# Optimization experiments

Measured on AMD Instinct MI355X. Metric: run time of the kernel, lower is better.

The kernel has to match this reference:

```python
import jax, jax.numpy as jnp
import numpy as np

B, N, E, F_IN, F_OUT = 2, 50000, 800000, 128, 128


def setup_inputs() -> dict:
    key = jax.random.key(0)
    k1, k2, k3, k4 = jax.random.split(key, 4)
    x = jax.random.normal(k1, (B, N, F_IN), dtype=jnp.float32)
    edge_index = jax.random.randint(k2, (2, E), 0, N, dtype=jnp.int64)
    edge_weight = jax.random.uniform(k3, (E,), dtype=jnp.float32)
    # Linear params (xavier_uniform weight, zero bias)
    limit = float(np.sqrt(6.0 / (F_IN + F_OUT)))
    W = jax.random.uniform(k4, (F_OUT, F_IN), minval=-limit, maxval=limit, dtype=jnp.float32)
    b = jnp.zeros((F_OUT,), dtype=jnp.float32)
    return {"x": x, "edge_index": edge_index, "edge_weight": edge_weight, "W": W, "b": b}


def reference(x, edge_index, edge_weight, W, b):
    src, dst = edge_index[0], edge_index[1]
    num_nodes = x.shape[1]
    # in-degree of dst, clamped to >= 1
    deg = jax.ops.segment_sum(jnp.ones_like(dst, dtype=x.dtype), dst, num_segments=num_nodes)
    deg_inv_sqrt = jnp.clip(deg, 1.0, None) ** -0.5
    norm = deg_inv_sqrt[src] * edge_weight * deg_inv_sqrt[dst]  # [E]

    def aggregate(xb):  # xb: [N, F]
        msg = xb[src] * norm[:, None]  # [E, F] gather + scale
        return jax.ops.segment_sum(msg, dst, num_segments=num_nodes)  # scatter-add

    out = jax.vmap(aggregate)(x)  # [B, N, F]
    return out @ W.T + b
```

## Files before the change

kernel.cpp:

```cpp
#include <hip/hip_runtime.h>
#include <hip/hip_fp16.h>

typedef unsigned int u32;
typedef unsigned short u16;
typedef __attribute__((ext_vector_type(8))) short bf16x8;
typedef __attribute__((ext_vector_type(4))) float f32x4;

#define WS_ALIGN(x) (((x) + 255) & ~(size_t)255)

__device__ inline u16 f2bf(float f) {
    u32 u = __float_as_uint(f);
    u32 r = (u + 0x7fffu + ((u >> 16) & 1u)) >> 16;
    return (u16)r;
}

__global__ void prep_kernel(const float* __restrict__ W, uint2* __restrict__ Wh,
                            int* __restrict__ deg, int N) {
    int t = blockIdx.x * 256 + threadIdx.x;
    if (t < N) deg[t] = 0;
    if (t < 4096) {
        float4 v = ((const float4*)W)[t];
        Wh[t] = make_uint2((u32)f2bf(v.x) | ((u32)f2bf(v.y) << 16),
                           (u32)f2bf(v.z) | ((u32)f2bf(v.w) << 16));
    }
}

__global__ __launch_bounds__(256) void front_kernel(const float* __restrict__ x,
                                                    const u16* __restrict__ Wh,
                                                    const int* __restrict__ dst,
                                                    int* __restrict__ deg,
                                                    u16* __restrict__ yh,
                                                    int N, int E, int gpb) {
    int bid = blockIdx.x;
    if (bid < 2 * gpb) {
        int b = (bid >= gpb) ? 1 : 0;
        int gb = bid - b * gpb;
        int wv = gb * 4 + (threadIdx.x >> 6);
        int r0 = wv * 32;
        if (r0 >= N) return;
        int lane = threadIdx.x & 63;
        int l15 = lane & 15, g = lane >> 4;

        bf16x8 xb[2][4];
#pragma unroll
        for (int m = 0; m < 2; ++m) {
            int xrow = r0 + m * 16 + l15;
            if (xrow >= N) xrow = N - 1;
            const float* xp = x + ((size_t)b * N + xrow) * 128 + g * 8;
#pragma unroll
            for (int kt = 0; kt < 4; ++kt) {
                float4 u0 = *(const float4*)(xp + kt * 32);
                float4 u1 = *(const float4*)(xp + kt * 32 + 4);
                bf16x8 t;
                t[0] = (short)f2bf(u0.x); t[1] = (short)f2bf(u0.y);
                t[2] = (short)f2bf(u0.z); t[3] = (short)f2bf(u0.w);
                t[4] = (short)f2bf(u1.x); t[5] = (short)f2bf(u1.y);
                t[6] = (short)f2bf(u1.z); t[7] = (short)f2bf(u1.w);
                xb[m][kt] = t;
            }
        }

        int n0 = r0 + l15, n1 = r0 + 16 + l15;
        u16* yp0 = yh + (size_t)n0 * 256 + b * 128 + g * 4;
        u16* yp1 = yh + (size_t)n1 * 256 + b * 128 + g * 4;
#pragma unroll
        for (int ct = 0; ct < 8; ++ct) {
            const u16* wp = Wh + (size_t)(ct * 16 + l15) * 128 + g * 8;
            f32x4 a0 = {0.f, 0.f, 0.f, 0.f};
            f32x4 a1 = {0.f, 0.f, 0.f, 0.f};
#pragma unroll
            for (int kt = 0; kt < 4; ++kt) {
                bf16x8 wf = *(const bf16x8*)(wp + kt * 32);
                a0 = __builtin_amdgcn_mfma_f32_16x16x32_bf16(wf, xb[0][kt], a0, 0, 0, 0);
                a1 = __builtin_amdgcn_mfma_f32_16x16x32_bf16(wf, xb[1][kt], a1, 0, 0, 0);
            }
            if (n0 < N) {
                u32 lo = (u32)f2bf(a0[0]) | ((u32)f2bf(a0[1]) << 16);
                u32 hi = (u32)f2bf(a0[2]) | ((u32)f2bf(a0[3]) << 16);
                *(uint2*)(yp0 + ct * 16) = make_uint2(lo, hi);
            }
            if (n1 < N) {
                u32 lo = (u32)f2bf(a1[0]) | ((u32)f2bf(a1[1]) << 16);
                u32 hi = (u32)f2bf(a1[2]) | ((u32)f2bf(a1[3]) << 16);
                *(uint2*)(yp1 + ct * 16) = make_uint2(lo, hi);
            }
        }
    } else {
        int e0 = ((bid - 2 * gpb) * 256 + threadIdx.x) * 4;
        if (e0 + 3 < E) {
            int4 d4 = *(const int4*)(dst + e0);
            atomicAdd(&deg[d4.x], 1);
            atomicAdd(&deg[d4.y], 1);
            atomicAdd(&deg[d4.z], 1);
            atomicAdd(&deg[d4.w], 1);
        } else {
            for (int e = e0; e < E; ++e) atomicAdd(&deg[dst[e]], 1);
        }
    }
}

__global__ void scan1_kernel(const int* __restrict__ deg, int* __restrict__ bsum, int N) {
    __shared__ int tmp[256];
    int tid = threadIdx.x;
    int i0 = blockIdx.x * 1024 + tid * 4;
    int s = 0;
    if (i0 + 3 < N) {
        int4 v = *(const int4*)(deg + i0);
        s = v.x + v.y + v.z + v.w;
    } else {
        for (int j = 0; j < 4; ++j) if (i0 + j < N) s += deg[i0 + j];
    }
    tmp[tid] = s;
    __syncthreads();
    for (int off = 1; off < 256; off <<= 1) {
        int t = (tid >= off) ? tmp[tid - off] : 0;
        __syncthreads();
        tmp[tid] += t;
        __syncthreads();
    }
    if (tid == 255) bsum[blockIdx.x] = tmp[255];
}

__global__ void scan3_kernel(const int* __restrict__ deg, const int* __restrict__ bsum,
                             int* __restrict__ rowptr, int* __restrict__ cursor,
                             float* __restrict__ dis, int N, int nb) {
    __shared__ int tmp[256];
    __shared__ int bs[256];
    int tid = threadIdx.x;
    bs[tid] = (tid < nb) ? bsum[tid] : 0;
    __syncthreads();
    for (int off = 1; off < 256; off <<= 1) {
        int t = (tid >= off) ? bs[tid - off] : 0;
        __syncthreads();
        bs[tid] += t;
        __syncthreads();
    }
    int boff = bs[blockIdx.x] - bsum[blockIdx.x];

    int i0 = blockIdx.x * 1024 + tid * 4;
    int4 v;
    if (i0 + 3 < N) {
        v = *(const int4*)(deg + i0);
    } else {
        v.x = (i0 < N) ? deg[i0] : 0;
        v.y = (i0 + 1 < N) ? deg[i0 + 1] : 0;
        v.z = (i0 + 2 < N) ? deg[i0 + 2] : 0;
        v.w = (i0 + 3 < N) ? deg[i0 + 3] : 0;
    }
    int s = v.x + v.y + v.z + v.w;
    tmp[tid] = s;
    __syncthreads();
    for (int off = 1; off < 256; off <<= 1) {
        int t = (tid >= off) ? tmp[tid - off] : 0;
        __syncthreads();
        tmp[tid] += t;
        __syncthreads();
    }
    int e0 = tmp[tid] - s + boff;
    int e1 = e0 + v.x, e2 = e1 + v.y, e3 = e2 + v.z;
    if (i0 < N) {
        rowptr[i0] = e0; cursor[i0] = e0;
        dis[i0] = rsqrtf((float)(v.x < 1 ? 1 : v.x));
        if (i0 == N - 1) rowptr[N] = e1;
    }
    if (i0 + 1 < N) {
        rowptr[i0 + 1] = e1; cursor[i0 + 1] = e1;
        dis[i0 + 1] = rsqrtf((float)(v.y < 1 ? 1 : v.y));
        if (i0 + 1 == N - 1) rowptr[N] = e2;
    }
    if (i0 + 2 < N) {
        rowptr[i0 + 2] = e2; cursor[i0 + 2] = e2;
        dis[i0 + 2] = rsqrtf((float)(v.z < 1 ? 1 : v.z));
        if (i0 + 2 == N - 1) rowptr[N] = e3;
    }
    if (i0 + 3 < N) {
        rowptr[i0 + 3] = e3; cursor[i0 + 3] = e3;
        dis[i0 + 3] = rsqrtf((float)(v.w < 1 ? 1 : v.w));
        if (i0 + 3 == N - 1) rowptr[N] = e3 + v.w;
    }
}

__global__ void fill_kernel(const int* __restrict__ src, const int* __restrict__ dst,
                            const float* __restrict__ ew, const float* __restrict__ dis,
                            int* __restrict__ cursor, u32* __restrict__ csr, int E) {
    int e0 = (blockIdx.x * blockDim.x + threadIdx.x) * 4;
    if (e0 + 3 < E) {
        int4 s4 = *(const int4*)(src + e0);
        int4 d4 = *(const int4*)(dst + e0);
        float4 w4 = *(const float4*)(ew + e0);
        {
            float nm = dis[s4.x] * w4.x * dis[d4.x];
            int pos = atomicAdd(&cursor[d4.x], 1);
            csr[pos] = ((u32)__half_as_ushort(__float2half_rn(nm)) << 16) | (u32)s4.x;
        }
        {
            float nm = dis[s4.y] * w4.y * dis[d4.y];
            int pos = atomicAdd(&cursor[d4.y], 1);
            csr[pos] = ((u32)__half_as_ushort(__float2half_rn(nm)) << 16) | (u32)s4.y;
        }
        {
            float nm = dis[s4.z] * w4.z * dis[d4.z];
            int pos = atomicAdd(&cursor[d4.z], 1);
            csr[pos] = ((u32)__half_as_ushort(__float2half_rn(nm)) << 16) | (u32)s4.z;
        }
        {
            float nm = dis[s4.w] * w4.w * dis[d4.w];
            int pos = atomicAdd(&cursor[d4.w], 1);
            csr[pos] = ((u32)__half_as_ushort(__float2half_rn(nm)) << 16) | (u32)s4.w;
        }
    } else {
        for (int e = e0; e < E; ++e) {
            int s = src[e], d = dst[e];
            float nm = dis[s] * ew[e] * dis[d];
            int pos = atomicAdd(&cursor[d], 1);
            csr[pos] = ((u32)__half_as_ushort(__float2half_rn(nm)) << 16) | (u32)s;
        }
    }
}

__global__ __launch_bounds__(64) void agg_kernel(const u32* __restrict__ yh,
                                                 const int* __restrict__ rowptr,
                                                 const u32* __restrict__ csr,
                                                 const float* __restrict__ bias,
                                                 float* __restrict__ out, int N) {
    int node = blockIdx.x;
    int b = blockIdx.y;
    int lane = threadIdx.x;
    const u32* xb = yh + (size_t)b * 64 + lane;
    int beg = rowptr[node], end = rowptr[node + 1];
    float2 acc = make_float2(0.f, 0.f);

    int j0 = beg;
    for (; j0 + 8 <= end; j0 += 8) {
        u32 pv[8];
#pragma unroll
        for (int j = 0; j < 8; ++j) pv[j] = csr[j0 + j];
        u32 q[8];
#pragma unroll
        for (int j = 0; j < 8; ++j) q[j] = xb[(size_t)(pv[j] & 0xffffu) * 128];
#pragma unroll
        for (int j = 0; j < 8; ++j) {
            float nm = __half2float(__ushort_as_half((u16)(pv[j] >> 16)));
            acc.x = fmaf(__uint_as_float(q[j] << 16), nm, acc.x);
            acc.y = fmaf(__uint_as_float(q[j] & 0xffff0000u), nm, acc.y);
        }
    }
    for (; j0 < end; ++j0) {
        u32 pv = csr[j0];
        float nm = __half2float(__ushort_as_half((u16)(pv >> 16)));
        u32 v = xb[(size_t)(pv & 0xffffu) * 128];
        acc.x = fmaf(__uint_as_float(v << 16), nm, acc.x);
        acc.y = fmaf(__uint_as_float(v & 0xffff0000u), nm, acc.y);
    }

    float2 bv = *(const float2*)(bias + lane * 2);
    acc.x += bv.x; acc.y += bv.y;
    *(float2*)(out + ((size_t)b * N + node) * 128 + lane * 2) = acc;
}

extern "C" void kernel_launch(void* const* d_in, const int* in_sizes, int n_in,
                              void* d_out, int out_size, void* d_ws, size_t ws_size,
                              hipStream_t stream) {
    const float* x    = (const float*)d_in[0];
    const int*   eidx = (const int*)d_in[1];
    const float* ew   = (const float*)d_in[2];
    const float* W    = (const float*)d_in[3];
    const float* bias = (const float*)d_in[4];
    float* out = (float*)d_out;

    const int E = in_sizes[2];
    const int N = in_sizes[0] / 256;
    const int nb = (N + 1023) / 1024;

    const int* src = eidx;
    const int* dst = eidx + E;

    char* w = (char*)d_ws;
    int*   deg    = (int*)w;   w += WS_ALIGN((size_t)N * 4);
    int*   rowptr = (int*)w;   w += WS_ALIGN((size_t)(N + 1) * 4);
    int*   cursor = (int*)w;   w += WS_ALIGN((size_t)N * 4);
    float* dis    = (float*)w; w += WS_ALIGN((size_t)N * 4);
    int*   bsum   = (int*)w;   w += WS_ALIGN((size_t)nb * 4);
    u32*   csr    = (u32*)w;   w += WS_ALIGN((size_t)E * 4);
    u16*   yh     = (u16*)w;   w += WS_ALIGN((size_t)N * 512);
    uint2* Wh     = (uint2*)w; w += WS_ALIGN((size_t)128 * 128 * 2);

    int pgrid = (N > 4096 ? N : 4096);
    hipLaunchKernelGGL(prep_kernel, dim3((pgrid + 255) / 256), dim3(256), 0, stream,
                       W, Wh, deg, N);
    int gpb = ((N + 31) / 32 + 3) / 4;
    int degBlocks = ((E + 3) / 4 + 255) / 256;
    hipLaunchKernelGGL(front_kernel, dim3(2 * gpb + degBlocks), dim3(256), 0, stream,
                       x, (const u16*)Wh, dst, deg, yh, N, E, gpb);
    hipLaunchKernelGGL(scan1_kernel, dim3(nb), dim3(256), 0, stream, deg, bsum, N);
    hipLaunchKernelGGL(scan3_kernel, dim3(nb), dim3(256), 0, stream, deg, bsum, rowptr, cursor, dis, N, nb);
    hipLaunchKernelGGL(fill_kernel, dim3(((E + 3) / 4 + 255) / 256), dim3(256), 0, stream,
                       src, dst, ew, dis, cursor, csr, E);
    hipLaunchKernelGGL(agg_kernel,  dim3(N, 2), dim3(64), 0, stream,
                       (const u32*)yh, rowptr, csr, bias, out, N);
}
```

Measured before the change: 164.5 us.

## Pad degree counters to stride 8, reuse as cursor, split GEMM from degree count

Degree counters are padded to one counter per 32 bytes to spread atomic contention across cache lines. The padded array is then reused as the CSR fill cursor, which removes the separate cursor array. The fused GEMM/degree kernel is split into separate gemm and deg kernels, and zeroing moves from prep_kernel to a memset. This adds a launch and an 8x larger footprint for strided scan reads, and gives up the overlap of atomics with MFMA work that the fused kernel had.

```diff
diff --git a/kernel.cpp b/kernel.cpp
--- a/kernel.cpp
+++ b/kernel.cpp
@@ -7,6 +7,7 @@
 typedef __attribute__((ext_vector_type(4))) float f32x4;
 
 #define WS_ALIGN(x) (((x) + 255) & ~(size_t)255)
+#define DEG_STRIDE 8
 
 __device__ inline u16 f2bf(float f) {
     u32 u = __float_as_uint(f);
@@ -14,10 +15,8 @@
     return (u16)r;
 }
 
-__global__ void prep_kernel(const float* __restrict__ W, uint2* __restrict__ Wh,
-                            int* __restrict__ deg, int N) {
+__global__ void prep_kernel(const float* __restrict__ W, uint2* __restrict__ Wh) {
     int t = blockIdx.x * 256 + threadIdx.x;
-    if (t < N) deg[t] = 0;
     if (t < 4096) {
         float4 v = ((const float4*)W)[t];
         Wh[t] = make_uint2((u32)f2bf(v.x) | ((u32)f2bf(v.y) << 16),
@@ -25,91 +24,85 @@
     }
 }
 
-__global__ __launch_bounds__(256) void front_kernel(const float* __restrict__ x,
-                                                    const u16* __restrict__ Wh,
-                                                    const int* __restrict__ dst,
-                                                    int* __restrict__ deg,
-                                                    u16* __restrict__ yh,
-                                                    int N, int E, int gpb) {
+__global__ __launch_bounds__(256) void gemm_kernel(const float* __restrict__ x,
+                                                   const u16* __restrict__ Wh,
+                                                   u16* __restrict__ yh,
+                                                   int N, int gpb) {
     int bid = blockIdx.x;
-    if (bid < 2 * gpb) {
-        int b = (bid >= gpb) ? 1 : 0;
-        int gb = bid - b * gpb;
-        int wv = gb * 4 + (threadIdx.x >> 6);
-        int r0 = wv * 32;
-        if (r0 >= N) return;
-        int lane = threadIdx.x & 63;
-        int l15 = lane & 15, g = lane >> 4;
-
-        bf16x8 xb[2][4];
-#pragma unroll
-        for (int m = 0; m < 2; ++m) {
-            int xrow = r0 + m * 16 + l15;
-            if (xrow >= N) xrow = N - 1;
-            const float* xp = x + ((size_t)b * N + xrow) * 128 + g * 8;
-#pragma unroll
-            for (int kt = 0; kt < 4; ++kt) {
-                float4 u0 = *(const float4*)(xp + kt * 32);
-                float4 u1 = *(const float4*)(xp + kt * 32 + 4);
-                bf16x8 t;
-                t[0] = (short)f2bf(u0.x); t[1] = (short)f2bf(u0.y);
-                t[2] = (short)f2bf(u0.z); t[3] = (short)f2bf(u0.w);
-                t[4] = (short)f2bf(u1.x); t[5] = (short)f2bf(u1.y);
-                t[6] = (short)f2bf(u1.z); t[7] = (short)f2bf(u1.w);
-                xb[m][kt] = t;
-            }
-        }
-
-        int n0 = r0 + l15, n1 = r0 + 16 + l15;
-        u16* yp0 = yh + (size_t)n0 * 256 + b * 128 + g * 4;
-        u16* yp1 = yh + (size_t)n1 * 256 + b * 128 + g * 4;
-#pragma unroll
-        for (int ct = 0; ct < 8; ++ct) {
-            const u16* wp = Wh + (size_t)(ct * 16 + l15) * 128 + g * 8;
-            f32x4 a0 = {0.f, 0.f, 0.f, 0.f};
-            f32x4 a1 = {0.f, 0.f, 0.f, 0.f};
-#pragma unroll
-            for (int kt = 0; kt < 4; ++kt) {
-                bf16x8 wf = *(const bf16x8*)(wp + kt * 32);
-                a0 = __builtin_amdgcn_mfma_f32_16x16x32_bf16(wf, xb[0][kt], a0, 0, 0, 0);
-                a1 = __builtin_amdgcn_mfma_f32_16x16x32_bf16(wf, xb[1][kt], a1, 0, 0, 0);
-            }
-            if (n0 < N) {
-                u32 lo = (u32)f2bf(a0[0]) | ((u32)f2bf(a0[1]) << 16);
-                u32 hi = (u32)f2bf(a0[2]) | ((u32)f2bf(a0[3]) << 16);
-                *(uint2*)(yp0 + ct * 16) = make_uint2(lo, hi);
-            }
-            if (n1 < N) {
-                u32 lo = (u32)f2bf(a1[0]) | ((u32)f2bf(a1[1]) << 16);
-                u32 hi = (u32)f2bf(a1[2]) | ((u32)f2bf(a1[3]) << 16);
-                *(uint2*)(yp1 + ct * 16) = make_uint2(lo, hi);
-            }
-        }
+    int b = (bid >= gpb) ? 1 : 0;
+    int gb = bid - b * gpb;
+    int wv = gb * 4 + (threadIdx.x >> 6);
+    int r0 = wv * 32;
+    if (r0 >= N) return;
+    int lane = threadIdx.x & 63;
+    int l15 = lane & 15, g = lane >> 4;
+
+    bf16x8 xb[2][4];
+#pragma unroll
+    for (int m = 0; m < 2; ++m) {
+        int xrow = r0 + m * 16 + l15;
+        if (xrow >= N) xrow = N - 1;
+        const float* xp = x + ((size_t)b * N + xrow) * 128 + g * 8;
+#pragma unroll
+        for (int kt = 0; kt < 4; ++kt) {
+            float4 u0 = *(const float4*)(xp + kt * 32);
+            float4 u1 = *(const float4*)(xp + kt * 32 + 4);
+            bf16x8 t;
+            t[0] = (short)f2bf(u0.x); t[1] = (short)f2bf(u0.y);
+            t[2] = (short)f2bf(u0.z); t[3] = (short)f2bf(u0.w);
+            t[4] = (short)f2bf(u1.x); t[5] = (short)f2bf(u1.y);
+            t[6] = (short)f2bf(u1.z); t[7] = (short)f2bf(u1.w);
+            xb[m][kt] = t;
+        }
+    }
+
+    int n0 = r0 + l15, n1 = r0 + 16 + l15;
+    u16* yp0 = yh + (size_t)n0 * 256 + b * 128 + g * 4;
+    u16* yp1 = yh + (size_t)n1 * 256 + b * 128 + g * 4;
+#pragma unroll
+    for (int ct = 0; ct < 8; ++ct) {
+        const u16* wp = Wh + (size_t)(ct * 16 + l15) * 128 + g * 8;
+        f32x4 a0 = {0.f, 0.f, 0.f, 0.f};
+        f32x4 a1 = {0.f, 0.f, 0.f, 0.f};
+#pragma unroll
+        for (int kt = 0; kt < 4; ++kt) {
+            bf16x8 wf = *(const bf16x8*)(wp + kt * 32);
+            a0 = __builtin_amdgcn_mfma_f32_16x16x32_bf16(wf, xb[0][kt], a0, 0, 0, 0);
+            a1 = __builtin_amdgcn_mfma_f32_16x16x32_bf16(wf, xb[1][kt], a1, 0, 0, 0);
+        }
+        if (n0 < N) {
+            u32 lo = (u32)f2bf(a0[0]) | ((u32)f2bf(a0[1]) << 16);
+            u32 hi = (u32)f2bf(a0[2]) | ((u32)f2bf(a0[3]) << 16);
+            *(uint2*)(yp0 + ct * 16) = make_uint2(lo, hi);
+        }
+        if (n1 < N) {
+            u32 lo = (u32)f2bf(a1[0]) | ((u32)f2bf(a1[1]) << 16);
+            u32 hi = (u32)f2bf(a1[2]) | ((u32)f2bf(a1[3]) << 16);
+            *(uint2*)(yp1 + ct * 16) = make_uint2(lo, hi);
+        }
+    }
+}
+
+__global__ void deg_kernel(const int* __restrict__ dst, int* __restrict__ degp, int E) {
+    int e0 = (blockIdx.x * blockDim.x + threadIdx.x) * 4;
+    if (e0 + 3 < E) {
+        int4 d4 = *(const int4*)(dst + e0);
+        atomicAdd(&degp[d4.x * DEG_STRIDE], 1);
+        atomicAdd(&degp[d4.y * DEG_STRIDE], 1);
+        atomicAdd(&degp[d4.z * DEG_STRIDE], 1);
+        atomicAdd(&degp[d4.w * DEG_STRIDE], 1);
     } else {
-        int e0 = ((bid - 2 * gpb) * 256 + threadIdx.x) * 4;
-        if (e0 + 3 < E) {
-            int4 d4 = *(const int4*)(dst + e0);
-            atomicAdd(&deg[d4.x], 1);
-            atomicAdd(&deg[d4.y], 1);
-            atomicAdd(&deg[d4.z], 1);
-            atomicAdd(&deg[d4.w], 1);
-        } else {
-            for (int e = e0; e < E; ++e) atomicAdd(&deg[dst[e]], 1);
-        }
-    }
-}
-
-__global__ void scan1_kernel(const int* __restrict__ deg, int* __restrict__ bsum, int N) {
+        for (int e = e0; e < E; ++e) atomicAdd(&degp[dst[e] * DEG_STRIDE], 1);
+    }
+}
+
+__global__ void scan1_kernel(const int* __restrict__ degp, int* __restrict__ bsum, int N) {
     __shared__ int tmp[256];
     int tid = threadIdx.x;
     int i0 = blockIdx.x * 1024 + tid * 4;
     int s = 0;
-    if (i0 + 3 < N) {
-        int4 v = *(const int4*)(deg + i0);
-        s = v.x + v.y + v.z + v.w;
-    } else {
-        for (int j = 0; j < 4; ++j) if (i0 + j < N) s += deg[i0 + j];
-    }
+#pragma unroll
+    for (int j = 0; j < 4; ++j) if (i0 + j < N) s += degp[(i0 + j) * DEG_STRIDE];
     tmp[tid] = s;
     __syncthreads();
     for (int off = 1; off < 256; off <<= 1) {
@@ -121,9 +114,9 @@
     if (tid == 255) bsum[blockIdx.x] = tmp[255];
 }
 
-__global__ void scan3_kernel(const int* __restrict__ deg, const int* __restrict__ bsum,
-                             int* __restrict__ rowptr, int* __restrict__ cursor,
-                             float* __restrict__ dis, int N, int nb) {
+__global__ void scan3_kernel(int* __restrict__ degp, const int* __restrict__ bsum,
+                             int* __restrict__ rowptr, float* __restrict__ dis,
+                             int N, int nb) {
     __shared__ int tmp[256];
     __shared__ int bs[256];
     int tid = threadIdx.x;
@@ -138,16 +131,11 @@
     int boff = bs[blockIdx.x] - bsum[blockIdx.x];
 
     int i0 = blockIdx.x * 1024 + tid * 4;
-    int4 v;
-    if (i0 + 3 < N) {
-        v = *(const int4*)(deg + i0);
-    } else {
-        v.x = (i0 < N) ? deg[i0] : 0;
-        v.y = (i0 + 1 < N) ? deg[i0 + 1] : 0;
-        v.z = (i0 + 2 < N) ? deg[i0 + 2] : 0;
-        v.w = (i0 + 3 < N) ? deg[i0 + 3] : 0;
-    }
-    int s = v.x + v.y + v.z + v.w;
+    int v0 = (i0 < N) ? degp[i0 * DEG_STRIDE] : 0;
+    int v1 = (i0 + 1 < N) ? degp[(i0 + 1) * DEG_STRIDE] : 0;
+    int v2 = (i0 + 2 < N) ? degp[(i0 + 2) * DEG_STRIDE] : 0;
+    int v3 = (i0 + 3 < N) ? degp[(i0 + 3) * DEG_STRIDE] : 0;
+    int s = v0 + v1 + v2 + v3;
     tmp[tid] = s;
     __syncthreads();
     for (int off = 1; off < 256; off <<= 1) {
@@ -157,32 +145,32 @@
         __syncthreads();
     }
     int e0 = tmp[tid] - s + boff;
-    int e1 = e0 + v.x, e2 = e1 + v.y, e3 = e2 + v.z;
+    int e1 = e0 + v0, e2 = e1 + v1, e3 = e2 + v2;
     if (i0 < N) {
-        rowptr[i0] = e0; cursor[i0] = e0;
-        dis[i0] = rsqrtf((float)(v.x < 1 ? 1 : v.x));
+        rowptr[i0] = e0; degp[i0 * DEG_STRIDE] = e0;
+        dis[i0] = rsqrtf((float)(v0 < 1 ? 1 : v0));
         if (i0 == N - 1) rowptr[N] = e1;
     }
     if (i0 + 1 < N) {
-        rowptr[i0 + 1] = e1; cursor[i0 + 1] = e1;
-        dis[i0 + 1] = rsqrtf((float)(v.y < 1 ? 1 : v.y));
+        rowptr[i0 + 1] = e1; degp[(i0 + 1) * DEG_STRIDE] = e1;
+        dis[i0 + 1] = rsqrtf((float)(v1 < 1 ? 1 : v1));
         if (i0 + 1 == N - 1) rowptr[N] = e2;
     }
     if (i0 + 2 < N) {
-        rowptr[i0 + 2] = e2; cursor[i0 + 2] = e2;
-        dis[i0 + 2] = rsqrtf((float)(v.z < 1 ? 1 : v.z));
+        rowptr[i0 + 2] = e2; degp[(i0 + 2) * DEG_STRIDE] = e2;
+        dis[i0 + 2] = rsqrtf((float)(v2 < 1 ? 1 : v2));
         if (i0 + 2 == N - 1) rowptr[N] = e3;
     }
     if (i0 + 3 < N) {
-        rowptr[i0 + 3] = e3; cursor[i0 + 3] = e3;
-        dis[i0 + 3] = rsqrtf((float)(v.w < 1 ? 1 : v.w));
-        if (i0 + 3 == N - 1) rowptr[N] = e3 + v.w;
+        rowptr[i0 + 3] = e3; degp[(i0 + 3) * DEG_STRIDE] = e3;
+        dis[i0 + 3] = rsqrtf((float)(v3 < 1 ? 1 : v3));
+        if (i0 + 3 == N - 1) rowptr[N] = e3 + v3;
     }
 }
 
 __global__ void fill_kernel(const int* __restrict__ src, const int* __restrict__ dst,
                             const float* __restrict__ ew, const float* __restrict__ dis,
-                            int* __restrict__ cursor, u32* __restrict__ csr, int E) {
+                            int* __restrict__ degp, u32* __restrict__ csr, int E) {
     int e0 = (blockIdx.x * blockDim.x + threadIdx.x) * 4;
     if (e0 + 3 < E) {
         int4 s4 = *(const int4*)(src + e0);
@@ -190,29 +178,29 @@
         float4 w4 = *(const float4*)(ew + e0);
         {
             float nm = dis[s4.x] * w4.x * dis[d4.x];
-            int pos = atomicAdd(&cursor[d4.x], 1);
+            int pos = atomicAdd(&degp[d4.x * DEG_STRIDE], 1);
             csr[pos] = ((u32)__half_as_ushort(__float2half_rn(nm)) << 16) | (u32)s4.x;
         }
         {
             float nm = dis[s4.y] * w4.y * dis[d4.y];
-            int pos = atomicAdd(&cursor[d4.y], 1);
+            int pos = atomicAdd(&degp[d4.y * DEG_STRIDE], 1);
             csr[pos] = ((u32)__half_as_ushort(__float2half_rn(nm)) << 16) | (u32)s4.y;
         }
         {
             float nm = dis[s4.z] * w4.z * dis[d4.z];
-            int pos = atomicAdd(&cursor[d4.z], 1);
+            int pos = atomicAdd(&degp[d4.z * DEG_STRIDE], 1);
             csr[pos] = ((u32)__half_as_ushort(__float2half_rn(nm)) << 16) | (u32)s4.z;
         }
         {
             float nm = dis[s4.w] * w4.w * dis[d4.w];
-            int pos = atomicAdd(&cursor[d4.w], 1);
+            int pos = atomicAdd(&degp[d4.w * DEG_STRIDE], 1);
             csr[pos] = ((u32)__half_as_ushort(__float2half_rn(nm)) << 16) | (u32)s4.w;
         }
     } else {
         for (int e = e0; e < E; ++e) {
             int s = src[e], d = dst[e];
             float nm = dis[s] * ew[e] * dis[d];
-            int pos = atomicAdd(&cursor[d], 1);
+            int pos = atomicAdd(&degp[d * DEG_STRIDE], 1);
             csr[pos] = ((u32)__half_as_ushort(__float2half_rn(nm)) << 16) | (u32)s;
         }
     }
@@ -276,26 +264,25 @@
     const int* dst = eidx + E;
 
     char* w = (char*)d_ws;
-    int*   deg    = (int*)w;   w += WS_ALIGN((size_t)N * 4);
+    int*   degp   = (int*)w;   w += WS_ALIGN((size_t)N * DEG_STRIDE * 4);
     int*   rowptr = (int*)w;   w += WS_ALIGN((size_t)(N + 1) * 4);
-    int*   cursor = (int*)w;   w += WS_ALIGN((size_t)N * 4);
     float* dis    = (float*)w; w += WS_ALIGN((size_t)N * 4);
     int*   bsum   = (int*)w;   w += WS_ALIGN((size_t)nb * 4);
     u32*   csr    = (u32*)w;   w += WS_ALIGN((size_t)E * 4);
     u16*   yh     = (u16*)w;   w += WS_ALIGN((size_t)N * 512);
     uint2* Wh     = (uint2*)w; w += WS_ALIGN((size_t)128 * 128 * 2);
 
-    int pgrid = (N > 4096 ? N : 4096);
-    hipLaunchKernelGGL(prep_kernel, dim3((pgrid + 255) / 256), dim3(256), 0, stream,
-                       W, Wh, deg, N);
+    hipMemsetAsync(degp, 0, (size_t)N * DEG_STRIDE * 4, stream);
+    hipLaunchKernelGGL(prep_kernel, dim3(16), dim3(256), 0, stream, W, Wh);
     int gpb = ((N + 31) / 32 + 3) / 4;
-    int degBlocks = ((E + 3) / 4 + 255) / 256;
-    hipLaunchKernelGGL(front_kernel, dim3(2 * gpb + degBlocks), dim3(256), 0, stream,
-                       x, (const u16*)Wh, dst, deg, yh, N, E, gpb);
-    hipLaunchKernelGGL(scan1_kernel, dim3(nb), dim3(256), 0, stream, deg, bsum, N);
-    hipLaunchKernelGGL(scan3_kernel, dim3(nb), dim3(256), 0, stream, deg, bsum, rowptr, cursor, dis, N, nb);
+    hipLaunchKernelGGL(gemm_kernel, dim3(2 * gpb), dim3(256), 0, stream,
+                       x, (const u16*)Wh, yh, N, gpb);
+    hipLaunchKernelGGL(deg_kernel, dim3(((E + 3) / 4 + 255) / 256), dim3(256), 0, stream,
+                       dst, degp, E);
+    hipLaunchKernelGGL(scan1_kernel, dim3(nb), dim3(256), 0, stream, degp, bsum, N);
+    hipLaunchKernelGGL(scan3_kernel, dim3(nb), dim3(256), 0, stream, degp, bsum, rowptr, dis, N, nb);
     hipLaunchKernelGGL(fill_kernel, dim3(((E + 3) / 4 + 255) / 256), dim3(256), 0, stream,
-                       src, dst, ew, dis, cursor, csr, E);
+                       src, dst, ew, dis, degp, csr, E);
     hipLaunchKernelGGL(agg_kernel,  dim3(N, 2), dim3(64), 0, stream,
                        (const u32*)yh, rowptr, csr, bias, out, N);
 }
```

After: 175.0 us. +6.4%, slower.
